# Kernel tuning notes

Measured on AMD Instinct MI355X. Metric: run time of the kernel, lower is better.

The kernel has to match this reference:

```python
import jax, jax.numpy as jnp
import numpy as np

B, S, d, D = 128, 1024, 64, 64  # batch, seq_len, physical dim, bond dim


def setup_inputs() -> dict:
    key = jax.random.key(0)
    k1, k2, k3, k4 = jax.random.split(key, 4)
    k_core = (d * D * D) ** (-0.5)
    k_vec = d ** (-0.5)
    core = k_core * jax.random.normal(k1, (d, D, D), dtype=jnp.float32)
    left_boundary = k_vec * jax.random.normal(k2, (D,), dtype=jnp.float32)
    right_boundary = k_vec * jax.random.normal(k3, (D,), dtype=jnp.float32)
    X = jax.random.randint(k4, (B, S), 0, d, dtype=jnp.int32)
    return {"X": X, "core": core, "left_boundary": left_boundary,
            "right_boundary": right_boundary}


def reference(X, core, left_boundary, right_boundary):
    """Faithful JAX version of TTrain._log_contract_at_batch (homogeneous).

    X: [B, S] int category indices; core: [d, D, D]; boundaries: [D].
    Returns logprobs: [B].
    The per-step normalization (infinity-norm) + accumulated log-norm trick of
    the original is preserved exactly; the final
    log((exp(lognorm) * out)**2) is computed in the mathematically identical
    stable form 2*(lognorm + log|out|).
    """
    batch = X.shape[0]
    lb = jnp.broadcast_to(left_boundary, (batch, left_boundary.shape[0]))  # [B, D]
    Z0 = jnp.max(jnp.abs(lb), axis=1)                                      # [B]
    c0 = lb / Z0[:, None]
    logn0 = jnp.log(Z0)

    def step(carry, x_t):
        c, logn = carry                       # c: [B, D]
        w_t = core[x_t]                       # gather selected cores: [B, D, D]
        ct = jnp.einsum('bi,bij->bj', c, w_t)  # [B, D]
        Zt = jnp.max(jnp.abs(ct), axis=1)      # [B] infinity norm
        return (ct / Zt[:, None], logn + jnp.log(Zt)), None

    (c, logn), _ = jax.lax.scan(step, (c0, logn0), X.T)  # scan over seq axis
    out = jnp.einsum('bi,i->b', c, right_boundary)        # [B]
    logprobs = 2.0 * (logn + jnp.log(jnp.abs(out)))
    return logprobs
```

## Files before the change

### kernel.cpp

```cpp
#include <hip/hip_runtime.h>
#include <math.h>


#define TT_S 1024
#define TT_D 64

typedef __attribute__((ext_vector_type(8))) short short8;
typedef __attribute__((ext_vector_type(4))) float float4v;
typedef __attribute__((ext_vector_type(2))) unsigned int uint2v;

__device__ __forceinline__ unsigned bf16_rne(float f) {
    unsigned u = __float_as_uint(f);
    return (u + 0x7FFFu + ((u >> 16) & 1u)) >> 16;
}

__global__ __launch_bounds__(64) void tt_prep(
    const float* __restrict__ core, short* __restrict__ tblA,
    short* __restrict__ tblB)
{
    const int x = blockIdx.x, l = threadIdx.x;
    const int n = l & 15, q = l >> 4;
    const float* W = core + x * 4096;
    #pragma unroll
    for (int I = 0; I < 4; ++I)
        #pragma unroll
        for (int Kp = 0; Kp < 2; ++Kp) {
            short8 v;
            const int row = 16 * I + n, k0 = 32 * Kp + 8 * q;
            #pragma unroll
            for (int j = 0; j < 8; ++j) v[j] = (short)bf16_rne(W[row * 64 + k0 + j]);
            *(short8*)(tblA + ((size_t)(x * 8 + I * 2 + Kp) * 64 + l) * 8) = v;
        }
    #pragma unroll
    for (int Kp = 0; Kp < 2; ++Kp)
        #pragma unroll
        for (int J = 0; J < 4; ++J) {
            short8 v;
            const int col = 16 * J + n, k0 = 32 * Kp + 8 * q;
            #pragma unroll
            for (int j = 0; j < 8; ++j) v[j] = (short)bf16_rne(W[(k0 + j) * 64 + col]);
            *(short8*)(tblB + ((size_t)(x * 8 + Kp * 4 + J) * 64 + l) * 8) = v;
        }
}

__global__ __launch_bounds__(64, 2) void tt_stage1(
    const int* __restrict__ X, const short* __restrict__ tblA,
    const short* __restrict__ tblB, float* __restrict__ PT,
    float* __restrict__ ln1)
{
    __shared__ short mt[64 * 72];
    const int w = blockIdx.x;
    const int b = w >> 4, chunk = w & 15;
    const int l = threadIdx.x, n = l & 15, q = l >> 4;
    const int t0 = chunk * 64;
    const int xv = X[b * TT_S + t0 + l];

    short8 Bf[8];
    {
        const int x63 = __builtin_amdgcn_readfirstlane(__shfl(xv, 63));
        const short8* p = (const short8*)(tblB + (size_t)x63 * 4096 + l * 8);
        #pragma unroll
        for (int f = 0; f < 8; ++f) Bf[f] = p[f * 64];
    }
    float4v acc[4][4];
    float logn = 0.f;
    const float4v zero = {0.f, 0.f, 0.f, 0.f};

    #pragma unroll 1
    for (int s = 0; s < 63; ++s) {
        const int t = 62 - s;
        const int xt = __builtin_amdgcn_readfirstlane(__shfl(xv, t));
        const short8* pa = (const short8*)(tblA + (size_t)xt * 4096 + l * 8);
        short8 Af[8];
        #pragma unroll
        for (int f = 0; f < 8; ++f) Af[f] = pa[f * 64];

        if (s > 0) {
            if ((s & 7) == 0) {
                float Z = 0.f;
                #pragma unroll
                for (int I = 0; I < 4; ++I)
                    #pragma unroll
                    for (int J = 0; J < 4; ++J)
                        #pragma unroll
                        for (int r = 0; r < 4; ++r)
                            Z = fmaxf(Z, fabsf(acc[I][J][r]));
                #pragma unroll
                for (int m = 32; m; m >>= 1) Z = fmaxf(Z, __shfl_xor(Z, m));
                logn += logf(Z);
                const float rZ = 1.0f / Z;
                #pragma unroll
                for (int I = 0; I < 4; ++I)
                    #pragma unroll
                    for (int J = 0; J < 4; ++J)
                        #pragma unroll
                        for (int r = 0; r < 4; ++r) acc[I][J][r] *= rZ;
            }
            #pragma unroll
            for (int I = 0; I < 4; ++I)
                #pragma unroll
                for (int J = 0; J < 4; ++J) {
                    const float4v v = acc[I][J];
                    uint2v dd;
                    dd[0] = __builtin_amdgcn_perm(__float_as_uint(v[1]),
                                                  __float_as_uint(v[0]), 0x07060302u);
                    dd[1] = __builtin_amdgcn_perm(__float_as_uint(v[3]),
                                                  __float_as_uint(v[2]), 0x07060302u);
                    *(uint2v*)(mt + (16 * J + n) * 72 + 16 * I + 4 * q) = dd;
                }
            asm volatile("s_waitcnt lgkmcnt(0)" ::: "memory");
            #pragma unroll
            for (int Kp = 0; Kp < 2; ++Kp)
                #pragma unroll
                for (int J = 0; J < 4; ++J)
                    Bf[Kp * 4 + J] =
                        *(const short8*)(mt + (16 * J + n) * 72 + 32 * Kp + 8 * q);
        }

        #pragma unroll
        for (int I = 0; I < 4; ++I)
            #pragma unroll
            for (int J = 0; J < 4; ++J) {
                float4v c0 = __builtin_amdgcn_mfma_f32_16x16x32_bf16(
                    Af[I * 2 + 0], Bf[0 * 4 + J], zero, 0, 0, 0);
                acc[I][J] = __builtin_amdgcn_mfma_f32_16x16x32_bf16(
                    Af[I * 2 + 1], Bf[1 * 4 + J], c0, 0, 0, 0);
            }
    }

    {
        float Z = 0.f;
        #pragma unroll
        for (int I = 0; I < 4; ++I)
            #pragma unroll
            for (int J = 0; J < 4; ++J)
                #pragma unroll
                for (int r = 0; r < 4; ++r) Z = fmaxf(Z, fabsf(acc[I][J][r]));
        #pragma unroll
        for (int m = 32; m; m >>= 1) Z = fmaxf(Z, __shfl_xor(Z, m));
        logn += logf(Z);
        const float rZ = 1.0f / Z;
        float* base = PT + (size_t)w * 4096;
        #pragma unroll
        for (int I = 0; I < 4; ++I)
            #pragma unroll
            for (int J = 0; J < 4; ++J) {
                float4v v = acc[I][J];
                #pragma unroll
                for (int r = 0; r < 4; ++r) v[r] *= rZ;
                *(float4v*)(base + (16 * J + n) * 64 + 16 * I + 4 * q) = v;
            }
        if (l == 0) ln1[w] = logn;
    }
}

__global__ __launch_bounds__(64) void tt_stage2(
    const float* __restrict__ PT, const float* __restrict__ ln1,
    const float* __restrict__ lb, const float* __restrict__ rb,
    float* __restrict__ out)
{
    __shared__ float cb[64];
    const int b = blockIdx.x, j = threadIdx.x;

    float c = lb[j];
    float Z = fabsf(c);
    #pragma unroll
    for (int m = 32; m; m >>= 1) Z = fmaxf(Z, __shfl_xor(Z, m));
    float logn = logf(Z);
    c *= (1.0f / Z);

    float ln = (j < 16) ? ln1[b * 16 + j] : 0.f;
    #pragma unroll
    for (int m = 32; m; m >>= 1) ln += __shfl_xor(ln, m);
    logn += ln;

    const float* base = PT + (size_t)b * 16 * 4096 + j * 64;
    float4v wb[16];
    #pragma unroll
    for (int f = 0; f < 16; ++f) wb[f] = ((const float4v*)base)[f];

    #pragma unroll 1
    for (int k = 0; k < 16; ++k) {
        float4v wn[16];
        const float4v* nb = (const float4v*)(base + (size_t)((k + 1) & 15) * 4096);
        #pragma unroll
        for (int f = 0; f < 16; ++f) wn[f] = nb[f];

        cb[j] = c;
        asm volatile("s_waitcnt lgkmcnt(0)" ::: "memory");
        float a0 = 0.f, a1 = 0.f, a2 = 0.f, a3 = 0.f;
        #pragma unroll
        for (int f = 0; f < 16; ++f) {
            const float4v cv = *(const float4v*)(cb + 4 * f);
            a0 = fmaf(cv[0], wb[f][0], a0);
            a1 = fmaf(cv[1], wb[f][1], a1);
            a2 = fmaf(cv[2], wb[f][2], a2);
            a3 = fmaf(cv[3], wb[f][3], a3);
        }
        float cn = (a0 + a1) + (a2 + a3);
        float Zl = fabsf(cn);
        #pragma unroll
        for (int m = 32; m; m >>= 1) Zl = fmaxf(Zl, __shfl_xor(Zl, m));
        logn += logf(Zl);
        c = cn * (1.0f / Zl);
        #pragma unroll
        for (int f = 0; f < 16; ++f) wb[f] = wn[f];
    }

    float dot = c * rb[j];
    #pragma unroll
    for (int m = 32; m; m >>= 1) dot += __shfl_xor(dot, m);
    if (j == 0) out[b] = 2.0f * (logn + logf(fabsf(dot)));
}

__global__ __launch_bounds__(256) void tt_transpose(
    const float* __restrict__ core, float* __restrict__ coreT)
{
    __shared__ float tile[64][65];
    const int x = blockIdx.x;
    const float* src = core + x * 4096;
    float* dst = coreT + x * 4096;
    const int r0 = threadIdx.x >> 6, cc = threadIdx.x & 63;
    #pragma unroll
    for (int k = 0; k < 16; ++k) tile[r0 + 4 * k][cc] = src[(r0 + 4 * k) * 64 + cc];
    __syncthreads();
    #pragma unroll
    for (int k = 0; k < 16; ++k) dst[(r0 + 4 * k) * 64 + cc] = tile[cc][r0 + 4 * k];
}

__global__ __launch_bounds__(64, 1) void ttrain_chain2(
    const int* __restrict__ X, const float* __restrict__ coreT,
    const float* __restrict__ lb, const float* __restrict__ rb,
    float* __restrict__ out)
{
    __shared__ float cbuf[2][64];
    const int b = blockIdx.x, j = threadIdx.x;
    const int* Xrow = X + b * TT_S;
    float c = lb[j];
    float Z = fabsf(c);
    #pragma unroll
    for (int m = 32; m; m >>= 1) Z = fmaxf(Z, __shfl_xor(Z, m));
    float logn = logf(Z);
    c *= (1.0f / Z);
    const float* colbase = coreT + j * 64;
    int xs_cur = Xrow[j];
    int xs_nxt = Xrow[64 + j];
    float4 wA[16], wB[16];
    {
        const int x0 = Xrow[0];
        const float4* p = (const float4*)(colbase + x0 * 4096);
        #pragma unroll
        for (int k = 0; k < 16; ++k) wA[k] = p[k];
    }
    #define TT_STEP(WCUR, WNXT, SLOT, XNEXT, T)                              \
    {                                                                        \
        cbuf[SLOT][j] = c;                                                   \
        {                                                                    \
            const float4* pre = (const float4*)(colbase + (XNEXT) * 4096);   \
            _Pragma("unroll")                                                \
            for (int k = 0; k < 16; ++k) WNXT[k] = pre[k];                   \
        }                                                                    \
        asm volatile("s_waitcnt lgkmcnt(0)" ::: "memory");                   \
        float a0 = 0.f, a1 = 0.f, a2 = 0.f, a3 = 0.f;                        \
        const float4* cb2 = (const float4*)cbuf[SLOT];                       \
        _Pragma("unroll")                                                    \
        for (int k = 0; k < 16; ++k) {                                       \
            float4 cv = cb2[k];                                              \
            a0 = fmaf(cv.x, WCUR[k].x, a0);                                  \
            a1 = fmaf(cv.y, WCUR[k].y, a1);                                  \
            a2 = fmaf(cv.z, WCUR[k].z, a2);                                  \
            a3 = fmaf(cv.w, WCUR[k].w, a3);                                  \
        }                                                                    \
        float cn = (a0 + a1) + (a2 + a3);                                    \
        if (((T) & 7) == 7) {                                                \
            float Zl = fabsf(cn);                                            \
            _Pragma("unroll")                                                \
            for (int m = 32; m; m >>= 1) Zl = fmaxf(Zl, __shfl_xor(Zl, m));  \
            logn += logf(Zl);                                                \
            cn *= (1.0f / Zl);                                               \
        }                                                                    \
        c = cn;                                                              \
    }
    for (int tc = 0; tc < TT_S; tc += 64) {
        #pragma unroll 1
        for (int u = 0; u < 64; u += 2) {
            const int x1 = __builtin_amdgcn_readlane(xs_cur, u + 1);
            TT_STEP(wA, wB, 0, x1, tc + u)
            const int src2 = (u + 2 < 64) ? xs_cur : xs_nxt;
            const int x2 = __builtin_amdgcn_readlane(src2, (u + 2) & 63);
            TT_STEP(wB, wA, 1, x2, tc + u + 1)
        }
        xs_cur = xs_nxt;
        const int nc = tc + 128;
        xs_nxt = Xrow[((nc < TT_S) ? nc : 0) + j];
    }
    #undef TT_STEP
    float dot = c * rb[j];
    #pragma unroll
    for (int m = 32; m; m >>= 1) dot += __shfl_xor(dot, m);
    if (j == 0) out[b] = 2.0f * (logn + logf(fabsf(dot)));
}

extern "C" void kernel_launch(void* const* d_in, const int* in_sizes, int n_in,
                              void* d_out, int out_size, void* d_ws, size_t ws_size,
                              hipStream_t stream) {
    const int*   X    = (const int*)d_in[0];
    const float* core = (const float*)d_in[1];
    const float* lb   = (const float*)d_in[2];
    const float* rb   = (const float*)d_in[3];
    float* out = (float*)d_out;

    const int B = in_sizes[0] / TT_S;
    const size_t tblBytes = (size_t)64 * 8 * 64 * 8 * sizeof(short);
    const size_t ptBytes  = (size_t)B * 16 * 4096 * sizeof(float);
    const size_t lnBytes  = (size_t)B * 16 * sizeof(float);
    const size_t need = 2 * tblBytes + ptBytes + lnBytes;

    if (ws_size >= need) {
        char* w = (char*)d_ws;
        short* tblA = (short*)w;
        short* tblB = (short*)(w + tblBytes);
        float* PT   = (float*)(w + 2 * tblBytes);
        float* ln1  = (float*)(w + 2 * tblBytes + ptBytes);
        tt_prep<<<64, 64, 0, stream>>>(core, tblA, tblB);
        tt_stage1<<<B * 16, 64, 0, stream>>>(X, tblA, tblB, PT, ln1);
        tt_stage2<<<B, 64, 0, stream>>>(PT, ln1, lb, rb, out);
    } else if (ws_size >= (size_t)64 * 4096 * sizeof(float)) {
        float* coreT = (float*)d_ws;
        tt_transpose<<<64, 256, 0, stream>>>(core, coreT);
        ttrain_chain2<<<B, TT_D, 0, stream>>>(X, coreT, lb, rb, out);
    }
}
```

Before: 155.0 us.

## Permute K index in core tables to keep MFMA output in registers, double-buffer A loads

The core tables are rebuilt with a permuted K ordering, so each MFMA accumulator tile can be packed straight into the next B operand with byte perms. This removes the LDS write, wait and read round trip in every chain step. A-fragment loads are double-buffered across two register sets so global loads overlap the MFMAs. bf16 conversion switches from round-to-nearest to truncation, which lowers accuracy slightly, and the extra buffers raise register pressure.

```diff
diff --git a/kernel.cpp b/kernel.cpp
--- a/kernel.cpp
+++ b/kernel.cpp
@@ -7,28 +7,32 @@
 
 typedef __attribute__((ext_vector_type(8))) short short8;
 typedef __attribute__((ext_vector_type(4))) float float4v;
-typedef __attribute__((ext_vector_type(2))) unsigned int uint2v;
-
-__device__ __forceinline__ unsigned bf16_rne(float f) {
-    unsigned u = __float_as_uint(f);
-    return (u + 0x7FFFu + ((u >> 16) & 1u)) >> 16;
+typedef __attribute__((ext_vector_type(4))) unsigned uint4v;
+
+static __device__ __forceinline__ short8 as_short8(uint4v u) {
+    union { uint4v u; short8 s; } x; x.u = u; return x.s;
 }
 
 __global__ __launch_bounds__(64) void tt_prep(
     const float* __restrict__ core, short* __restrict__ tblA,
-    short* __restrict__ tblB)
+    short* __restrict__ tblBt)
 {
     const int x = blockIdx.x, l = threadIdx.x;
     const int n = l & 15, q = l >> 4;
     const float* W = core + x * 4096;
+
     #pragma unroll
     for (int I = 0; I < 4; ++I)
         #pragma unroll
         for (int Kp = 0; Kp < 2; ++Kp) {
             short8 v;
-            const int row = 16 * I + n, k0 = 32 * Kp + 8 * q;
+            const int row = 16 * I + n;
+            const int c0 = 32 * Kp + 4 * q;
             #pragma unroll
-            for (int j = 0; j < 8; ++j) v[j] = (short)bf16_rne(W[row * 64 + k0 + j]);
+            for (int j = 0; j < 8; ++j) {
+                const int col = c0 + 16 * (j >> 2) + (j & 3);
+                v[j] = (short)(__float_as_uint(W[row * 64 + col]) >> 16);
+            }
             *(short8*)(tblA + ((size_t)(x * 8 + I * 2 + Kp) * 64 + l) * 8) = v;
         }
     #pragma unroll
@@ -36,96 +40,111 @@
         #pragma unroll
         for (int J = 0; J < 4; ++J) {
             short8 v;
-            const int col = 16 * J + n, k0 = 32 * Kp + 8 * q;
+            const int col = 16 * J + n;
+            const int r0 = 32 * Kp + 4 * q;
             #pragma unroll
-            for (int j = 0; j < 8; ++j) v[j] = (short)bf16_rne(W[(k0 + j) * 64 + col]);
-            *(short8*)(tblB + ((size_t)(x * 8 + Kp * 4 + J) * 64 + l) * 8) = v;
+            for (int j = 0; j < 8; ++j) {
+                const int row = r0 + 16 * (j >> 2) + (j & 3);
+                v[j] = (short)(__float_as_uint(W[row * 64 + col]) >> 16);
+            }
+            *(short8*)(tblBt + ((size_t)(x * 8 + Kp * 4 + J) * 64 + l) * 8) = v;
         }
 }
 
 __global__ __launch_bounds__(64, 2) void tt_stage1(
     const int* __restrict__ X, const short* __restrict__ tblA,
-    const short* __restrict__ tblB, float* __restrict__ PT,
+    const short* __restrict__ tblBt, float* __restrict__ PT,
     float* __restrict__ ln1)
 {
-    __shared__ short mt[64 * 72];
     const int w = blockIdx.x;
     const int b = w >> 4, chunk = w & 15;
     const int l = threadIdx.x, n = l & 15, q = l >> 4;
-    const int t0 = chunk * 64;
-    const int xv = X[b * TT_S + t0 + l];
-
-    short8 Bf[8];
-    {
-        const int x63 = __builtin_amdgcn_readfirstlane(__shfl(xv, 63));
-        const short8* p = (const short8*)(tblB + (size_t)x63 * 4096 + l * 8);
-        #pragma unroll
-        for (int f = 0; f < 8; ++f) Bf[f] = p[f * 64];
-    }
+    const int* Xc = X + b * TT_S + chunk * 64;
+
+    const float4v zero = {0.f, 0.f, 0.f, 0.f};
     float4v acc[4][4];
+    short8 Bf[8], A0[8], A1[8];
     float logn = 0.f;
-    const float4v zero = {0.f, 0.f, 0.f, 0.f};
+
+    #define LOAD_FRAGS(DST, TBL, XIDX)                                        \
+    {   const short8* p_ = (const short8*)((TBL) + (size_t)(XIDX) * 4096) + l; \
+        _Pragma("unroll")                                                     \
+        for (int f_ = 0; f_ < 8; ++f_) (DST)[f_] = p_[f_ * 64]; }
+
+    #define MFMA_ALL(ABUF)                                                    \
+        _Pragma("unroll")                                                     \
+        for (int I_ = 0; I_ < 4; ++I_)                                        \
+            _Pragma("unroll")                                                 \
+            for (int J_ = 0; J_ < 4; ++J_) {                                  \
+                float4v c0_ = __builtin_amdgcn_mfma_f32_16x16x32_bf16(        \
+                    (ABUF)[2 * I_ + 0], Bf[J_], zero, 0, 0, 0);               \
+                acc[I_][J_] = __builtin_amdgcn_mfma_f32_16x16x32_bf16(        \
+                    (ABUF)[2 * I_ + 1], Bf[4 + J_], c0_, 0, 0, 0);            \
+            }
+
+    #define PACK_BF()                                                         \
+        _Pragma("unroll")                                                     \
+        for (int Kp_ = 0; Kp_ < 2; ++Kp_)                                     \
+            _Pragma("unroll")                                                 \
+            for (int J_ = 0; J_ < 4; ++J_) {                                  \
+                uint4v u_;                                                    \
+                u_[0] = __builtin_amdgcn_perm(                                \
+                    __float_as_uint(acc[2 * Kp_][J_][1]),                     \
+                    __float_as_uint(acc[2 * Kp_][J_][0]), 0x07060302u);       \
+                u_[1] = __builtin_amdgcn_perm(                                \
+                    __float_as_uint(acc[2 * Kp_][J_][3]),                     \
+                    __float_as_uint(acc[2 * Kp_][J_][2]), 0x07060302u);       \
+                u_[2] = __builtin_amdgcn_perm(                                \
+                    __float_as_uint(acc[2 * Kp_ + 1][J_][1]),                 \
+                    __float_as_uint(acc[2 * Kp_ + 1][J_][0]), 0x07060302u);   \
+                u_[3] = __builtin_amdgcn_perm(                                \
+                    __float_as_uint(acc[2 * Kp_ + 1][J_][3]),                 \
+                    __float_as_uint(acc[2 * Kp_ + 1][J_][2]), 0x07060302u);   \
+                Bf[Kp_ * 4 + J_] = as_short8(u_);                             \
+            }
+
+    #define RENORM()                                                          \
+    {   float Z_ = 0.f;                                                       \
+        _Pragma("unroll")                                                     \
+        for (int I_ = 0; I_ < 4; ++I_)                                        \
+            _Pragma("unroll")                                                 \
+            for (int J_ = 0; J_ < 4; ++J_)                                    \
+                _Pragma("unroll")                                             \
+                for (int r_ = 0; r_ < 4; ++r_)                                \
+                    Z_ = fmaxf(Z_, fabsf(acc[I_][J_][r_]));                   \
+        _Pragma("unroll")                                                     \
+        for (int m_ = 32; m_; m_ >>= 1) Z_ = fmaxf(Z_, __shfl_xor(Z_, m_));   \
+        logn += logf(Z_);                                                     \
+        const float rZ_ = 1.0f / Z_;                                          \
+        _Pragma("unroll")                                                     \
+        for (int I_ = 0; I_ < 4; ++I_)                                        \
+            _Pragma("unroll")                                                 \
+            for (int J_ = 0; J_ < 4; ++J_)                                    \
+                _Pragma("unroll")                                             \
+                for (int r_ = 0; r_ < 4; ++r_) acc[I_][J_][r_] *= rZ_; }
+
+    LOAD_FRAGS(Bf, tblBt, Xc[63])
+    LOAD_FRAGS(A0, tblA, Xc[62])
+    LOAD_FRAGS(A1, tblA, Xc[61])
+
+    MFMA_ALL(A0)
+    LOAD_FRAGS(A0, tblA, Xc[60])
 
     #pragma unroll 1
-    for (int s = 0; s < 63; ++s) {
-        const int t = 62 - s;
-        const int xt = __builtin_amdgcn_readfirstlane(__shfl(xv, t));
-        const short8* pa = (const short8*)(tblA + (size_t)xt * 4096 + l * 8);
-        short8 Af[8];
-        #pragma unroll
-        for (int f = 0; f < 8; ++f) Af[f] = pa[f * 64];
-
-        if (s > 0) {
-            if ((s & 7) == 0) {
-                float Z = 0.f;
-                #pragma unroll
-                for (int I = 0; I < 4; ++I)
-                    #pragma unroll
-                    for (int J = 0; J < 4; ++J)
-                        #pragma unroll
-                        for (int r = 0; r < 4; ++r)
-                            Z = fmaxf(Z, fabsf(acc[I][J][r]));
-                #pragma unroll
-                for (int m = 32; m; m >>= 1) Z = fmaxf(Z, __shfl_xor(Z, m));
-                logn += logf(Z);
-                const float rZ = 1.0f / Z;
-                #pragma unroll
-                for (int I = 0; I < 4; ++I)
-                    #pragma unroll
-                    for (int J = 0; J < 4; ++J)
-                        #pragma unroll
-                        for (int r = 0; r < 4; ++r) acc[I][J][r] *= rZ;
-            }
-            #pragma unroll
-            for (int I = 0; I < 4; ++I)
-                #pragma unroll
-                for (int J = 0; J < 4; ++J) {
-                    const float4v v = acc[I][J];
-                    uint2v dd;
-                    dd[0] = __builtin_amdgcn_perm(__float_as_uint(v[1]),
-                                                  __float_as_uint(v[0]), 0x07060302u);
-                    dd[1] = __builtin_amdgcn_perm(__float_as_uint(v[3]),
-                                                  __float_as_uint(v[2]), 0x07060302u);
-                    *(uint2v*)(mt + (16 * J + n) * 72 + 16 * I + 4 * q) = dd;
-                }
-            asm volatile("s_waitcnt lgkmcnt(0)" ::: "memory");
-            #pragma unroll
-            for (int Kp = 0; Kp < 2; ++Kp)
-                #pragma unroll
-                for (int J = 0; J < 4; ++J)
-                    Bf[Kp * 4 + J] =
-                        *(const short8*)(mt + (16 * J + n) * 72 + 32 * Kp + 8 * q);
-        }
-
-        #pragma unroll
-        for (int I = 0; I < 4; ++I)
-            #pragma unroll
-            for (int J = 0; J < 4; ++J) {
-                float4v c0 = __builtin_amdgcn_mfma_f32_16x16x32_bf16(
-                    Af[I * 2 + 0], Bf[0 * 4 + J], zero, 0, 0, 0);
-                acc[I][J] = __builtin_amdgcn_mfma_f32_16x16x32_bf16(
-                    Af[I * 2 + 1], Bf[1 * 4 + J], c0, 0, 0, 0);
-            }
+    for (int it = 0; it < 31; ++it) {
+        PACK_BF()
+        MFMA_ALL(A1)
+        {
+            const int tn = 59 - 2 * it;
+            LOAD_FRAGS(A1, tblA, Xc[tn < 0 ? 0 : tn])
+        }
+        if (((2 * it + 2) & 7) == 0) RENORM()
+        PACK_BF()
+        MFMA_ALL(A0)
+        {
+            const int tn = 58 - 2 * it;
+            LOAD_FRAGS(A0, tblA, Xc[tn < 0 ? 0 : tn])
+        }
     }
 
     {
@@ -152,6 +171,10 @@
             }
         if (l == 0) ln1[w] = logn;
     }
+    #undef LOAD_FRAGS
+    #undef MFMA_ALL
+    #undef PACK_BF
+    #undef RENORM
 }
 
 __global__ __launch_bounds__(64) void tt_stage2(
@@ -318,12 +341,12 @@
 
     if (ws_size >= need) {
         char* w = (char*)d_ws;
-        short* tblA = (short*)w;
-        short* tblB = (short*)(w + tblBytes);
-        float* PT   = (float*)(w + 2 * tblBytes);
-        float* ln1  = (float*)(w + 2 * tblBytes + ptBytes);
-        tt_prep<<<64, 64, 0, stream>>>(core, tblA, tblB);
-        tt_stage1<<<B * 16, 64, 0, stream>>>(X, tblA, tblB, PT, ln1);
+        short* tblA  = (short*)w;
+        short* tblBt = (short*)(w + tblBytes);
+        float* PT    = (float*)(w + 2 * tblBytes);
+        float* ln1   = (float*)(w + 2 * tblBytes + ptBytes);
+        tt_prep<<<64, 64, 0, stream>>>(core, tblA, tblBt);
+        tt_stage1<<<B * 16, 64, 0, stream>>>(X, tblA, tblBt, PT, ln1);
         tt_stage2<<<B, 64, 0, stream>>>(PT, ln1, lb, rb, out);
     } else if (ws_size >= (size_t)64 * 4096 * sizeof(float)) {
         float* coreT = (float*)d_ws;
```

New measurement: 143.8 us. 1.08x faster.
